# Optimization experiments

Measured on AMD Instinct MI355X. Metric: run time of the kernel, lower is better.

The kernel has to match this reference:

```python
import jax, jax.numpy as jnp
import numpy as np

VOCAB = 50257
EMBED = 512
HEADS = 16
DHEAD = 128
HID = HEADS * DHEAD  # 2048
B = 4096
S = 10  # 2 * window_size


def setup_inputs() -> dict:
    key = jax.random.key(0)
    ks = jax.random.split(key, 9)
    inv = 1.0 / np.sqrt(EMBED)
    return {
        "t": jax.random.randint(ks[0], (B,), 0, VOCAB, dtype=jnp.int32),
        "c": jax.random.randint(ks[1], (B, S), 0, VOCAB, dtype=jnp.int32),
        "emb": jax.random.normal(ks[2], (VOCAB, EMBED), dtype=jnp.float32),
        "Wq": jax.random.uniform(ks[3], (HID, EMBED), jnp.float32, -inv, inv),
        "bq": jax.random.uniform(ks[4], (HID,), jnp.float32, -inv, inv),
        "Wk": jax.random.uniform(ks[5], (HID, EMBED), jnp.float32, -inv, inv),
        "bk": jax.random.uniform(ks[6], (HID,), jnp.float32, -inv, inv),
        "Wv": jax.random.uniform(ks[7], (HID, EMBED), jnp.float32, -inv, inv),
        "bv": jax.random.uniform(ks[8], (HID,), jnp.float32, -inv, inv),
    }


def reference(t, c, emb, Wq, bq, Wk, bk, Wv, bv):
    target = emb[t]        # [B, E]
    context = emb[c]       # [B, S, E]
    # Q = W_Q(target) viewed as [B, H, Dh]
    Q = (target @ Wq.T + bq).reshape(B, HEADS, DHEAD)
    # K = W_K(context) viewed per token as [H, Dh]; scores Q[i] @ K_t -> [H, H]
    K = (context @ Wk.T + bk).reshape(B, S, HEADS, DHEAD)
    W = jnp.einsum("bpd,bsqd->bspq", Q, K) / np.sqrt(DHEAD)  # [B, S, H, H]
    W = jax.nn.softmax(W, axis=-1)
    V = (context @ Wv.T + bv).reshape(B, S, HEADS, DHEAD)
    tmp = jnp.einsum("bspq,bsqd->bspd", W, V).reshape(B, S, HID)
    context_vector = jnp.sum(tmp, axis=1)       # [B, HID]
    target_vector = target @ Wv.T + bv          # [B, HID]
    return target_vector, context_vector
```

## Files before the change

kernel.cpp:

```cpp
#include <hip/hip_runtime.h>
#include <stdint.h>

typedef __bf16 bf8 __attribute__((ext_vector_type(8)));
typedef float f4 __attribute__((ext_vector_type(4)));
typedef unsigned short us4 __attribute__((ext_vector_type(4)));
typedef unsigned short us8 __attribute__((ext_vector_type(8)));
typedef float fl4 __attribute__((ext_vector_type(4)));

#define NB 4096
#define NS 10
#define NE 512
#define NH 2048

__device__ __forceinline__ unsigned short f2bf(float f) {
    uint32_t u = __builtin_bit_cast(uint32_t, f);
    u += 0x7FFFu + ((u >> 16) & 1u);
    return (unsigned short)(u >> 16);
}
__device__ __forceinline__ __bf16 bfb(unsigned short u) { return __builtin_bit_cast(__bf16, u); }

__device__ __forceinline__ void gl_lds16(const void* g, void* l) {
    __builtin_amdgcn_global_load_lds((const __attribute__((address_space(1))) uint32_t*)g,
                                     (__attribute__((address_space(3))) uint32_t*)l, 16, 0, 0);
}

__global__ __launch_bounds__(256) void prep_kernel(
    const int* __restrict__ t, const int* __restrict__ c, const float* __restrict__ emb,
    const float* __restrict__ Wq, const float* __restrict__ Wk, const float* __restrict__ Wv,
    unsigned short* __restrict__ Xt, unsigned short* __restrict__ Xc,
    unsigned short* __restrict__ wQ, unsigned short* __restrict__ wK, unsigned short* __restrict__ wV)
{
    int v = blockIdx.x * 256 + threadIdx.x;
    const float* src;
    unsigned short* dst;
    if (v < 524288) {
        int e4 = v << 2; int row = e4 >> 9;
        src = emb + (size_t)t[row] * NE + (e4 & 511);
        dst = Xt + e4;
    } else if (v < 5767168) {
        int vv = v - 524288; int e4 = vv << 2; int row = e4 >> 9;
        src = emb + (size_t)c[row] * NE + (e4 & 511);
        dst = Xc + e4;
    } else {
        int vv = v - 5767168; int which = vv >> 18; int e4 = (vv & 262143) << 2;
        src = (which == 0 ? Wq : (which == 1 ? Wk : Wv)) + e4;
        dst = (which == 0 ? wQ : (which == 1 ? wK : wV)) + e4;
    }
    fl4 f = *(const fl4*)src;
    us4 o;
    o[0] = f2bf(f[0]); o[1] = f2bf(f[1]); o[2] = f2bf(f[2]); o[3] = f2bf(f[3]);
    *(us4*)dst = o;
}

__global__ __launch_bounds__(256, 2) void gemm_all(
    const unsigned short* __restrict__ Xt, const unsigned short* __restrict__ Xc,
    const unsigned short* __restrict__ wQ, const unsigned short* __restrict__ wK,
    const unsigned short* __restrict__ wV,
    const float* __restrict__ bq, const float* __restrict__ bk, const float* __restrict__ bv,
    unsigned short* __restrict__ Qb, unsigned short* __restrict__ Kb, unsigned short* __restrict__ Vb,
    float* __restrict__ TV)
{
    int oid = blockIdx.x;
    int id = (oid & 7) * 1408 + (oid >> 3);

    const unsigned short* A; const unsigned short* W; const float* bias;
    unsigned short* outb = nullptr; float* outf = nullptr;
    int tile;
    if (id < 512)       { A = Xt; W = wQ; bias = bq; outb = Qb; tile = id; }
    else if (id < 1024) { A = Xt; W = wV; bias = bv; outf = TV; tile = id - 512; }
    else if (id < 6144) { A = Xc; W = wK; bias = bk; outb = Kb; tile = id - 1024; }
    else                { A = Xc; W = wV; bias = bv; outb = Vb; tile = id - 6144; }
    int mt = tile >> 4, nt = tile & 15;
    int m0 = mt * 128, n0 = nt * 128;

    __shared__ unsigned short Asm[128 * 64];
    __shared__ unsigned short Bsm[128 * 64];

    int tid = threadIdx.x;
    int lane = tid & 63, wid = tid >> 6;
    int hi = lane >> 4, lo = lane & 15;
    int wm = (wid >> 1) * 64, wn = (wid & 1) * 64;

    f4 acc[4][4] = {};

    for (int ks = 0; ks < 8; ++ks) {
        int k0 = ks * 64;
        for (int i = 0; i < 4; ++i) {
            int ci = (i << 8) + tid;
            int row = ci >> 3, ch = ci & 7;
            const unsigned short* ga = A + (size_t)(m0 + row) * NE + k0 + ch * 8;
            gl_lds16(ga, Asm + ((i << 8) + (tid & ~63)) * 8);
        }
        for (int i = 0; i < 4; ++i) {
            int ci = (i << 8) + tid;
            int row = ci >> 3, ch = ci & 7;
            const unsigned short* gb = W + (size_t)(n0 + row) * NE + k0 + ch * 8;
            gl_lds16(gb, Bsm + ((i << 8) + (tid & ~63)) * 8);
        }
        __syncthreads();
        for (int kk = 0; kk < 2; ++kk) {
            bf8 a[4], b[4];
            for (int mi = 0; mi < 4; ++mi)
                a[mi] = *(const bf8*)&Asm[(wm + mi * 16 + lo) * 64 + kk * 32 + hi * 8];
            for (int ni = 0; ni < 4; ++ni)
                b[ni] = *(const bf8*)&Bsm[(wn + ni * 16 + lo) * 64 + kk * 32 + hi * 8];
            for (int mi = 0; mi < 4; ++mi)
                for (int ni = 0; ni < 4; ++ni)
                    acc[mi][ni] = __builtin_amdgcn_mfma_f32_16x16x32_bf16(a[mi], b[ni], acc[mi][ni], 0, 0, 0);
        }
        __syncthreads();
    }

    for (int mi = 0; mi < 4; ++mi)
        for (int ni = 0; ni < 4; ++ni) {
            int n = n0 + wn + ni * 16 + lo;
            float bb = bias[n];
            for (int r = 0; r < 4; ++r) {
                int m = m0 + wm + mi * 16 + hi * 4 + r;
                float vv = acc[mi][ni][r] + bb;
                if (outb) outb[(size_t)m * NH + n] = f2bf(vv);
                else      outf[(size_t)m * NH + n] = vv;
            }
        }
}

__global__ __launch_bounds__(256, 2) void attn_kernel(
    const unsigned short* __restrict__ Qb, const unsigned short* __restrict__ Kb,
    const unsigned short* __restrict__ Vb, float* __restrict__ CV)
{
    __shared__ unsigned short Vl[4][2048];
    int tid = threadIdx.x, lane = tid & 63, wid = tid >> 6;
    int hi = lane >> 4, lo = lane & 15;
    int b = blockIdx.x * 4 + wid;

    const unsigned short* qrow = Qb + (size_t)b * NH;
    bf8 qf[4];
    for (int kk = 0; kk < 4; ++kk)
        qf[kk] = *(const bf8*)&qrow[lo * 128 + kk * 32 + hi * 8];

    f4 acc[8] = {};
    const float sc = 0.08838834764831845f;

    for (int s = 0; s < NS; ++s) {
        const unsigned short* vrow = Vb + ((size_t)b * NS + s) * NH;
        const unsigned short* krow = Kb + ((size_t)b * NS + s) * NH;

        for (int it = 0; it < 4; ++it) {
            int cc = lane + 64 * it;
            int q_ = cc >> 4, rem = cc & 15, tt = rem >> 1, e = rem & 1;
            us8 d = *(const us8*)&vrow[cc * 8];
            *(us8*)&Vl[wid][tt * 256 + q_ * 16 + e * 8] = d;
        }

        f4 st = {};
        for (int kk = 0; kk < 4; ++kk) {
            bf8 kf = *(const bf8*)&krow[lo * 128 + kk * 32 + hi * 8];
            st = __builtin_amdgcn_mfma_f32_16x16x32_bf16(kf, qf[kk], st, 0, 0, 0);
        }
        float e0 = st[0] * sc, e1 = st[1] * sc, e2 = st[2] * sc, e3 = st[3] * sc;
        float mx = fmaxf(fmaxf(e0, e1), fmaxf(e2, e3));
        mx = fmaxf(mx, __shfl_xor(mx, 16));
        mx = fmaxf(mx, __shfl_xor(mx, 32));
        float w0 = __expf(e0 - mx), w1 = __expf(e1 - mx), w2 = __expf(e2 - mx), w3 = __expf(e3 - mx);
        float sm = w0 + w1 + w2 + w3;
        sm += __shfl_xor(sm, 16);
        sm += __shfl_xor(sm, 32);
        float inv = 1.0f / sm;

        bf8 ap;
        ap[0] = (__bf16)(w0 * inv); ap[1] = (__bf16)(w1 * inv);
        ap[2] = (__bf16)(w2 * inv); ap[3] = (__bf16)(w3 * inv);
        ap[4] = (__bf16)0.0f; ap[5] = (__bf16)0.0f; ap[6] = (__bf16)0.0f; ap[7] = (__bf16)0.0f;

        for (int tt = 0; tt < 8; ++tt) {
            const unsigned short* base = &Vl[wid][tt * 256 + hi * 64 + lo];
            bf8 bv_;
            bv_[0] = bfb(base[0]);  bv_[1] = bfb(base[16]);
            bv_[2] = bfb(base[32]); bv_[3] = bfb(base[48]);
            bv_[4] = (__bf16)0.0f; bv_[5] = (__bf16)0.0f; bv_[6] = (__bf16)0.0f; bv_[7] = (__bf16)0.0f;
            acc[tt] = __builtin_amdgcn_mfma_f32_16x16x32_bf16(ap, bv_, acc[tt], 0, 0, 0);
        }
    }

    float* out = CV + (size_t)b * NH;
    for (int tt = 0; tt < 8; ++tt)
        for (int r = 0; r < 4; ++r)
            out[(hi * 4 + r) * 128 + tt * 16 + lo] = acc[tt][r];
}

extern "C" void kernel_launch(void* const* d_in, const int* in_sizes, int n_in,
                              void* d_out, int out_size, void* d_ws, size_t ws_size,
                              hipStream_t stream) {
    const int*   t   = (const int*)d_in[0];
    const int*   c   = (const int*)d_in[1];
    const float* emb = (const float*)d_in[2];
    const float* Wq  = (const float*)d_in[3];
    const float* bq  = (const float*)d_in[4];
    const float* Wk  = (const float*)d_in[5];
    const float* bk  = (const float*)d_in[6];
    const float* Wv  = (const float*)d_in[7];
    const float* bv  = (const float*)d_in[8];
    float* out = (float*)d_out;

    char* ws = (char*)d_ws;
    unsigned short* Xt = (unsigned short*)(ws);
    unsigned short* Xc = (unsigned short*)(ws + 4194304);
    unsigned short* wQ = (unsigned short*)(ws + 46137344);
    unsigned short* wK = (unsigned short*)(ws + 48234496);
    unsigned short* wV = (unsigned short*)(ws + 50331648);
    unsigned short* Qb = (unsigned short*)(ws + 52428800);
    unsigned short* Kb = (unsigned short*)(ws + 69206016);
    unsigned short* Vb = (unsigned short*)(ws + 236978176);

    prep_kernel<<<25600, 256, 0, stream>>>(t, c, emb, Wq, Wk, Wv, Xt, Xc, wQ, wK, wV);
    gemm_all<<<11264, 256, 0, stream>>>(Xt, Xc, wQ, wK, wV, bq, bk, bv, Qb, Kb, Vb, out);
    attn_kernel<<<1024, 256, 0, stream>>>(Qb, Kb, Vb, out + (size_t)NB * NH);
}
```

Baseline: 493.6 us.

## Permute V layout in GEMM epilogue and pipeline attention over token pairs

The context-V GEMM now loads permuted weight rows and writes V in a d-major, head-interleaved layout. This lets the attention kernel copy V straight into LDS with async global-to-LDS loads and read contiguous 4-element fragments. The attention loop handles two context tokens per iteration, packing both softmax weight sets into the full K=32 MFMA operand instead of zero-padding half of it. It also prefetches the next pair's K and V while computing the current pair. The costs are doubled LDS per wave, more registers and scattered 2-byte stores in the V GEMM epilogue.

```diff
diff --git a/kernel.cpp b/kernel.cpp
--- a/kernel.cpp
+++ b/kernel.cpp
@@ -5,6 +5,8 @@
 typedef float f4 __attribute__((ext_vector_type(4)));
 typedef unsigned short us4 __attribute__((ext_vector_type(4)));
 typedef unsigned short us8 __attribute__((ext_vector_type(8)));
+typedef unsigned short u16x4 __attribute__((ext_vector_type(4)));
+typedef unsigned short u16x8 __attribute__((ext_vector_type(8)));
 typedef float fl4 __attribute__((ext_vector_type(4)));
 
 #define NB 4096
@@ -70,6 +72,7 @@
     else if (id < 1024) { A = Xt; W = wV; bias = bv; outf = TV; tile = id - 512; }
     else if (id < 6144) { A = Xc; W = wK; bias = bk; outb = Kb; tile = id - 1024; }
     else                { A = Xc; W = wV; bias = bv; outb = Vb; tile = id - 6144; }
+    bool vperm = (id >= 6144);
     int mt = tile >> 4, nt = tile & 15;
     int m0 = mt * 128, n0 = nt * 128;
 
@@ -94,7 +97,8 @@
         for (int i = 0; i < 4; ++i) {
             int ci = (i << 8) + tid;
             int row = ci >> 3, ch = ci & 7;
-            const unsigned short* gb = W + (size_t)(n0 + row) * NE + k0 + ch * 8;
+            int grow = vperm ? (((row >> 3) << 7) + (nt << 3) + (row & 7)) : (n0 + row);
+            const unsigned short* gb = W + (size_t)grow * NE + k0 + ch * 8;
             gl_lds16(gb, Bsm + ((i << 8) + (tid & ~63)) * 8);
         }
         __syncthreads();
@@ -111,79 +115,135 @@
         __syncthreads();
     }
 
-    for (int mi = 0; mi < 4; ++mi)
+    if (vperm) {
         for (int ni = 0; ni < 4; ++ni) {
-            int n = n0 + wn + ni * 16 + lo;
-            float bb = bias[n];
-            for (int r = 0; r < 4; ++r) {
-                int m = m0 + wm + mi * 16 + hi * 4 + r;
-                float vv = acc[mi][ni][r] + bb;
-                if (outb) outb[(size_t)m * NH + n] = f2bf(vv);
-                else      outf[(size_t)m * NH + n] = vv;
+            int ln = wn + ni * 16 + lo;
+            int q = ln >> 3, d = (nt << 3) + (ln & 7);
+            float bb = bias[q * 128 + d];
+            for (int mi = 0; mi < 4; ++mi)
+                for (int r = 0; r < 4; ++r) {
+                    int m = m0 + wm + mi * 16 + hi * 4 + r;
+                    outb[(size_t)m * NH + d * 16 + q] = f2bf(acc[mi][ni][r] + bb);
+                }
+        }
+    } else {
+        for (int mi = 0; mi < 4; ++mi)
+            for (int ni = 0; ni < 4; ++ni) {
+                int n = n0 + wn + ni * 16 + lo;
+                float bb = bias[n];
+                for (int r = 0; r < 4; ++r) {
+                    int m = m0 + wm + mi * 16 + hi * 4 + r;
+                    float vv = acc[mi][ni][r] + bb;
+                    if (outb) outb[(size_t)m * NH + n] = f2bf(vv);
+                    else      outf[(size_t)m * NH + n] = vv;
+                }
             }
-        }
-}
-
-__global__ __launch_bounds__(256, 2) void attn_kernel(
+    }
+}
+
+__global__ __launch_bounds__(256, 4) void attn_kernel(
     const unsigned short* __restrict__ Qb, const unsigned short* __restrict__ Kb,
     const unsigned short* __restrict__ Vb, float* __restrict__ CV)
 {
-    __shared__ unsigned short Vl[4][2048];
+    __shared__ unsigned short Vl[4][4096];
     int tid = threadIdx.x, lane = tid & 63, wid = tid >> 6;
     int hi = lane >> 4, lo = lane & 15;
     int b = blockIdx.x * 4 + wid;
+    unsigned short* Vlw = &Vl[wid][0];
 
     const unsigned short* qrow = Qb + (size_t)b * NH;
     bf8 qf[4];
+#pragma unroll
     for (int kk = 0; kk < 4; ++kk)
         qf[kk] = *(const bf8*)&qrow[lo * 128 + kk * 32 + hi * 8];
 
+    const unsigned short* Vbase = Vb + (size_t)b * NS * NH;
+    const unsigned short* Kbase = Kb + (size_t)b * NS * NH;
+
     f4 acc[8] = {};
     const float sc = 0.08838834764831845f;
 
-    for (int s = 0; s < NS; ++s) {
-        const unsigned short* vrow = Vb + ((size_t)b * NS + s) * NH;
-        const unsigned short* krow = Kb + ((size_t)b * NS + s) * NH;
-
-        for (int it = 0; it < 4; ++it) {
-            int cc = lane + 64 * it;
-            int q_ = cc >> 4, rem = cc & 15, tt = rem >> 1, e = rem & 1;
-            us8 d = *(const us8*)&vrow[cc * 8];
-            *(us8*)&Vl[wid][tt * 256 + q_ * 16 + e * 8] = d;
-        }
-
-        f4 st = {};
-        for (int kk = 0; kk < 4; ++kk) {
-            bf8 kf = *(const bf8*)&krow[lo * 128 + kk * 32 + hi * 8];
-            st = __builtin_amdgcn_mfma_f32_16x16x32_bf16(kf, qf[kk], st, 0, 0, 0);
-        }
-        float e0 = st[0] * sc, e1 = st[1] * sc, e2 = st[2] * sc, e3 = st[3] * sc;
+#pragma unroll
+    for (int it = 0; it < 8; ++it)
+        gl_lds16(Vbase + it * 512 + lane * 8, Vlw + it * 512);
+    bf8 kA[4], kB[4];
+#pragma unroll
+    for (int kk = 0; kk < 4; ++kk)
+        kA[kk] = *(const bf8*)&Kbase[lo * 128 + kk * 32 + hi * 8];
+
+#pragma unroll
+    for (int p = 0; p < 5; ++p) {
+        asm volatile("s_waitcnt vmcnt(0)" ::: "memory");
+        const unsigned short* kb1 = Kbase + (size_t)(2 * p + 1) * NH;
+#pragma unroll
+        for (int kk = 0; kk < 4; ++kk)
+            kB[kk] = *(const bf8*)&kb1[lo * 128 + kk * 32 + hi * 8];
+
+        f4 st0 = {}, st1 = {};
+#pragma unroll
+        for (int kk = 0; kk < 4; ++kk)
+            st0 = __builtin_amdgcn_mfma_f32_16x16x32_bf16(kA[kk], qf[kk], st0, 0, 0, 0);
+#pragma unroll
+        for (int kk = 0; kk < 4; ++kk)
+            st1 = __builtin_amdgcn_mfma_f32_16x16x32_bf16(kB[kk], qf[kk], st1, 0, 0, 0);
+
+        u16x4 r0[8], r1[8];
+#pragma unroll
+        for (int tt = 0; tt < 8; ++tt) {
+            r0[tt] = *(const u16x4*)&Vlw[tt * 256 + lo * 16 + hi * 4];
+            r1[tt] = *(const u16x4*)&Vlw[2048 + tt * 256 + lo * 16 + hi * 4];
+        }
+        asm volatile("s_waitcnt lgkmcnt(0)" ::: "memory");
+
+        if (p < 4) {
+            const unsigned short* vn = Vbase + (size_t)(2 * p + 2) * NH;
+            const unsigned short* kn = Kbase + (size_t)(2 * p + 2) * NH;
+#pragma unroll
+            for (int it = 0; it < 8; ++it)
+                gl_lds16(vn + it * 512 + lane * 8, Vlw + it * 512);
+#pragma unroll
+            for (int kk = 0; kk < 4; ++kk)
+                kA[kk] = *(const bf8*)&kn[lo * 128 + kk * 32 + hi * 8];
+        }
+
+        float e0 = st0[0] * sc, e1 = st0[1] * sc, e2 = st0[2] * sc, e3 = st0[3] * sc;
         float mx = fmaxf(fmaxf(e0, e1), fmaxf(e2, e3));
         mx = fmaxf(mx, __shfl_xor(mx, 16));
         mx = fmaxf(mx, __shfl_xor(mx, 32));
-        float w0 = __expf(e0 - mx), w1 = __expf(e1 - mx), w2 = __expf(e2 - mx), w3 = __expf(e3 - mx);
-        float sm = w0 + w1 + w2 + w3;
+        float a0 = __expf(e0 - mx), a1 = __expf(e1 - mx), a2 = __expf(e2 - mx), a3 = __expf(e3 - mx);
+        float sm = a0 + a1 + a2 + a3;
         sm += __shfl_xor(sm, 16);
         sm += __shfl_xor(sm, 32);
-        float inv = 1.0f / sm;
+        float inv0 = 1.0f / sm;
+
+        float f0 = st1[0] * sc, f1 = st1[1] * sc, f2 = st1[2] * sc, f3 = st1[3] * sc;
+        float my = fmaxf(fmaxf(f0, f1), fmaxf(f2, f3));
+        my = fmaxf(my, __shfl_xor(my, 16));
+        my = fmaxf(my, __shfl_xor(my, 32));
+        float b0 = __expf(f0 - my), b1 = __expf(f1 - my), b2 = __expf(f2 - my), b3 = __expf(f3 - my);
+        float sn = b0 + b1 + b2 + b3;
+        sn += __shfl_xor(sn, 16);
+        sn += __shfl_xor(sn, 32);
+        float inv1 = 1.0f / sn;
 
         bf8 ap;
-        ap[0] = (__bf16)(w0 * inv); ap[1] = (__bf16)(w1 * inv);
-        ap[2] = (__bf16)(w2 * inv); ap[3] = (__bf16)(w3 * inv);
-        ap[4] = (__bf16)0.0f; ap[5] = (__bf16)0.0f; ap[6] = (__bf16)0.0f; ap[7] = (__bf16)0.0f;
-
+        ap[0] = (__bf16)(a0 * inv0); ap[1] = (__bf16)(a1 * inv0);
+        ap[2] = (__bf16)(a2 * inv0); ap[3] = (__bf16)(a3 * inv0);
+        ap[4] = (__bf16)(b0 * inv1); ap[5] = (__bf16)(b1 * inv1);
+        ap[6] = (__bf16)(b2 * inv1); ap[7] = (__bf16)(b3 * inv1);
+
+#pragma unroll
         for (int tt = 0; tt < 8; ++tt) {
-            const unsigned short* base = &Vl[wid][tt * 256 + hi * 64 + lo];
-            bf8 bv_;
-            bv_[0] = bfb(base[0]);  bv_[1] = bfb(base[16]);
-            bv_[2] = bfb(base[32]); bv_[3] = bfb(base[48]);
-            bv_[4] = (__bf16)0.0f; bv_[5] = (__bf16)0.0f; bv_[6] = (__bf16)0.0f; bv_[7] = (__bf16)0.0f;
+            u16x8 cat = __builtin_shufflevector(r0[tt], r1[tt], 0, 1, 2, 3, 4, 5, 6, 7);
+            bf8 bv_ = __builtin_bit_cast(bf8, cat);
             acc[tt] = __builtin_amdgcn_mfma_f32_16x16x32_bf16(ap, bv_, acc[tt], 0, 0, 0);
         }
     }
 
     float* out = CV + (size_t)b * NH;
+#pragma unroll
     for (int tt = 0; tt < 8; ++tt)
+#pragma unroll
         for (int r = 0; r < 4; ++r)
             out[(hi * 4 + r) * 128 + tt * 16 + lo] = acc[tt][r];
 }
```

Result: slower. 607.8 us (+23.1%).
